# Kernel optimization log

Measured on AMD Instinct MI355X. Metric: run time of the kernel, lower is better.

## Reference

```python
import jax, jax.numpy as jnp
import numpy as np

B, C, H, W, T = 2, 96, 64, 64, 64
NH = 8  # num_heads
WS = 2  # window size per axis (2,2,2)


def setup_inputs() -> dict:
    key = jax.random.key(0)
    ks = jax.random.split(key, 9)
    s = lambda fan_in: 1.0 / np.sqrt(fan_in)
    return {
        "x": jax.random.normal(ks[0], (B, C, H, W, T), dtype=jnp.float32),
        # linear weights stored [in, out] (transposed vs torch nn.Linear)
        "qkv_w": jax.random.normal(ks[1], (C, 3 * C), dtype=jnp.float32) * s(C),
        "qkv_b": jax.random.normal(ks[2], (3 * C,), dtype=jnp.float32) * 0.01,
        "merge_w": jax.random.normal(ks[3], (C, C), dtype=jnp.float32) * s(C),
        "merge_b": jax.random.normal(ks[4], (C,), dtype=jnp.float32) * 0.01,
        "w1": jax.random.normal(ks[5], (2 * C, C), dtype=jnp.float32) * s(2 * C),
        "b1": jax.random.normal(ks[6], (C,), dtype=jnp.float32) * 0.01,
        "w2": jax.random.normal(ks[7], (C, C), dtype=jnp.float32) * s(C),
        "b2": jax.random.normal(ks[8], (C,), dtype=jnp.float32) * 0.01,
    }


def reference(x, qkv_w, qkv_b, merge_w, merge_b, w1, b1, w2, b2):
    b, c, h, w, t = x.shape
    hd = c // NH
    scale = hd ** -0.5
    n = WS * WS * WS  # 8 tokens per window

    xp = jnp.transpose(x, (0, 2, 3, 4, 1))  # [B,H,W,T,C]
    # window partition -> [B*nWin, 8, C]
    xw = xp.reshape(b, h // WS, WS, w // WS, WS, t // WS, WS, c)
    xw = jnp.transpose(xw, (0, 1, 3, 5, 2, 4, 6, 7)).reshape(-1, n, c)

    # windowed MHSA
    qkv = (xw @ qkv_w + qkv_b).reshape(-1, n, 3, NH, hd)
    q, k, v = jnp.moveaxis(qkv, 2, 0)  # each [Bw, n, NH, hd]
    attn = jax.nn.softmax(jnp.einsum('bnhd,bmhd->bhnm', q * scale, k), axis=-1)
    msg = jnp.einsum('bhnm,bmhd->bnhd', attn, v).reshape(-1, n, c)
    msg = msg @ merge_w + merge_b

    # window reverse -> [B,H,W,T,C]
    msg = msg.reshape(b, h // WS, w // WS, t // WS, WS, WS, WS, c)
    msg = jnp.transpose(msg, (0, 1, 4, 2, 5, 3, 6, 7)).reshape(b, h, w, t, c)

    # concat residual path + MLP (GELU exact, matching torch nn.GELU default)
    xt = xp.reshape(b, h * w * t, c)
    mt = msg.reshape(b, h * w * t, c)
    hmid = jax.nn.gelu(jnp.concatenate([xt, mt], axis=-1) @ w1 + b1, approximate=False)
    out = hmid @ w2 + b2
    return jnp.transpose(out.reshape(b, h, w, t, c), (0, 4, 1, 2, 3))
```

## Files before the change

kernel.cpp:

```cpp
#include <hip/hip_runtime.h>
#include <math.h>

typedef short bf16x8 __attribute__((ext_vector_type(8)));
typedef float f32x4 __attribute__((ext_vector_type(4)));

#define SCALE_Q 0.28867513459481287f

__device__ __forceinline__ ushort f2bf(float f) {
  union { float f; unsigned int i; } v; v.f = f;
  unsigned int x = v.i;
  return (ushort)((x + 0x7fffu + ((x >> 16) & 1u)) >> 16);
}
__device__ __forceinline__ float bf2f(ushort u) {
  union { unsigned int i; float f; } v; v.i = ((unsigned int)u) << 16; return v.f;
}
__device__ __forceinline__ float bfLo(unsigned int d) {
  union { unsigned int i; float f; } v; v.i = d << 16; return v.f;
}
__device__ __forceinline__ float bfHi(unsigned int d) {
  union { unsigned int i; float f; } v; v.i = d & 0xffff0000u; return v.f;
}

__global__ void swizzle_w(const float* __restrict__ qkv_w,
                          const float* __restrict__ merge_w,
                          const float* __restrict__ merge_b,
                          const float* __restrict__ w1,
                          const float* __restrict__ b1,
                          const float* __restrict__ w2,
                          ushort* __restrict__ ws) {
  int g = blockIdx.x * 256 + threadIdx.x;
  if (g < 6912) {
    int tile = g >> 6, lane = g & 63;
    float vals[8];
    if (tile < 54) {
      int rem = tile % 18;
      int c0 = (tile / 18) * 96 + (rem / 3) * 16, k0 = (rem % 3) * 32;
      int n = c0 + (lane & 15), kb = k0 + (lane >> 4) * 8;
      float s = (tile < 18) ? SCALE_Q : 1.0f;
#pragma unroll
      for (int j = 0; j < 8; ++j) vals[j] = qkv_w[(size_t)(kb + j) * 288 + n] * s;
    } else if (tile < 72) {
      int rem = tile - 54;
      int c0 = (rem / 3) * 16, k0 = (rem % 3) * 32;
      int n = c0 + (lane & 15), kb = k0 + (lane >> 4) * 8;
#pragma unroll
      for (int j = 0; j < 8; ++j) vals[j] = w1[(size_t)(kb + j) * 96 + n];
    } else if (tile < 90) {
      int rem = tile - 72;
      int c0 = (rem / 3) * 16, k0 = (rem % 3) * 32;
      int n = c0 + (lane & 15), kb = k0 + (lane >> 4) * 8;
      float acc[8] = {0, 0, 0, 0, 0, 0, 0, 0};
      for (int m = 0; m < 96; ++m) {
        float wr = w1[(size_t)(96 + m) * 96 + n];
#pragma unroll
        for (int j = 0; j < 8; ++j) acc[j] += merge_w[(size_t)(kb + j) * 96 + m] * wr;
      }
#pragma unroll
      for (int j = 0; j < 8; ++j) vals[j] = acc[j];
    } else {
      int rem = tile - 90;
      int c0 = (rem / 3) * 16, k0 = (rem % 3) * 32;
      int n = c0 + (lane & 15), kb = k0 + (lane >> 4) * 8;
#pragma unroll
      for (int j = 0; j < 8; ++j) vals[j] = w2[(size_t)(kb + j) * 96 + n];
    }
    ushort tmp[8];
#pragma unroll
    for (int j = 0; j < 8; ++j) tmp[j] = f2bf(vals[j]);
    *(uint4*)(ws + tile * 512 + lane * 8) = *(const uint4*)tmp;
  } else if (g < 7008) {
    int n = g - 6912;
    float s = b1[n];
    for (int m = 0; m < 96; ++m) s += merge_b[m] * w1[(size_t)(96 + m) * 96 + n];
    ((float*)(ws + 55296))[n] = s;
  }
}

#define KPAD 104
#define QPAD 68
#define OPAD 65
__global__ __launch_bounds__(256, 3) void swin_mfma(
    const float* __restrict__ x,
    const float* __restrict__ qkv_b, const float* __restrict__ b2,
    const ushort* __restrict__ wsw, float* __restrict__ out) {
  __shared__ __align__(16) ushort R[288 * QPAD];

  const int tid = threadIdx.x, bid = blockIdx.x;
  const int t0 = bid & 3, w0 = (bid >> 2) & 31, h0 = (bid >> 7) & 31, b = bid >> 12;
  const int lane = tid & 63, wave = tid >> 6;
  const int mrow = lane & 15, quad = lane >> 4;
  const int arow = (wave * 16 + mrow) * KPAD + quad * 8;
  const int tokb = wave * 16 + quad * 4;
  const float* foldb = (const float*)(wsw + 55296);

  for (int i = tid; i < 1536; i += 256) {
    int q = i & 3, dw = (i >> 2) & 1, dh = (i >> 3) & 1, c = i >> 4;
    size_t g = ((((size_t)b * 96 + c) * 64 + h0 * 2 + dh) * 64 + w0 * 2 + dw) * 64 + t0 * 16 + q * 4;
    float4 v = *(const float4*)(x + g);
    float vv[4] = {v.x, v.y, v.z, v.w};
    int base = dh * 4 + dw * 2;
#pragma unroll
    for (int j = 0; j < 4; ++j) {
      int tl = q * 4 + j;
      R[((tl >> 1) * 8 + base + (tl & 1)) * KPAD + c] = f2bf(vv[j]);
    }
  }
  __syncthreads();

  bf16x8 aX[3];
#pragma unroll
  for (int kt = 0; kt < 3; ++kt)
    aX[kt] = *(const bf16x8*)(R + arow + kt * 32);
  __syncthreads();

  for (int cn = 0; cn < 3; ++cn) {
#pragma unroll
    for (int nt = 0; nt < 6; ++nt) {
      int col = cn * 96 + nt * 16 + mrow;
      float bias = qkv_b[col];
      if (cn == 0) bias *= SCALE_Q;
      f32x4 acc = {bias, bias, bias, bias};
#pragma unroll
      for (int kt = 0; kt < 3; ++kt) {
        bf16x8 bf = *(const bf16x8*)(wsw + (size_t)(cn * 18 + nt * 3 + kt) * 512 + lane * 8);
        acc = __builtin_amdgcn_mfma_f32_16x16x32_bf16(aX[kt], bf, acc, 0, 0, 0);
      }
#pragma unroll
      for (int r = 0; r < 4; ++r) R[col * QPAD + tokb + r] = f2bf(acc[r]);
    }
  }
  __syncthreads();

  {
    const int win = tid >> 5, head = (tid >> 2) & 7, r2 = (tid & 3) * 2;
    const ushort* Qb = R + (head * 12) * QPAD + win * 8;
    const ushort* Kb = R + (96 + head * 12) * QPAD + win * 8;
    const ushort* Vb = R + (192 + head * 12) * QPAD + win * 8;
    float q0[12], q1[12];
#pragma unroll
    for (int d = 0; d < 12; ++d) {
      unsigned int qq = *(const unsigned int*)(Qb + d * QPAD + r2);
      q0[d] = bfLo(qq);
      q1[d] = bfHi(qq);
    }
    float s0[8] = {0, 0, 0, 0, 0, 0, 0, 0}, s1[8] = {0, 0, 0, 0, 0, 0, 0, 0};
#pragma unroll
    for (int d = 0; d < 12; ++d) {
      uint2 ka = *(const uint2*)(Kb + d * QPAD);
      uint2 kc = *(const uint2*)(Kb + d * QPAD + 4);
      float kf[8] = {bfLo(ka.x), bfHi(ka.x), bfLo(ka.y), bfHi(ka.y),
                     bfLo(kc.x), bfHi(kc.x), bfLo(kc.y), bfHi(kc.y)};
#pragma unroll
      for (int m = 0; m < 8; ++m) { s0[m] += q0[d] * kf[m]; s1[m] += q1[d] * kf[m]; }
    }
    float mx0 = fmaxf(fmaxf(fmaxf(s0[0], s0[1]), fmaxf(s0[2], s0[3])),
                      fmaxf(fmaxf(s0[4], s0[5]), fmaxf(s0[6], s0[7])));
    float mx1 = fmaxf(fmaxf(fmaxf(s1[0], s1[1]), fmaxf(s1[2], s1[3])),
                      fmaxf(fmaxf(s1[4], s1[5]), fmaxf(s1[6], s1[7])));
    float sum0 = 0.f, sum1 = 0.f;
#pragma unroll
    for (int m = 0; m < 8; ++m) {
      s0[m] = __expf(s0[m] - mx0); sum0 += s0[m];
      s1[m] = __expf(s1[m] - mx1); sum1 += s1[m];
    }
    float inv0 = 1.0f / sum0, inv1 = 1.0f / sum1;
    float o0[12], o1[12];
#pragma unroll
    for (int d = 0; d < 12; ++d) {
      uint2 va = *(const uint2*)(Vb + d * QPAD);
      uint2 vc = *(const uint2*)(Vb + d * QPAD + 4);
      float vf[8] = {bfLo(va.x), bfHi(va.x), bfLo(va.y), bfHi(va.y),
                     bfLo(vc.x), bfHi(vc.x), bfLo(vc.y), bfHi(vc.y)};
      float a0 = 0.f, a1 = 0.f;
#pragma unroll
      for (int m = 0; m < 8; ++m) { a0 += s0[m] * vf[m]; a1 += s1[m] * vf[m]; }
      o0[d] = a0 * inv0; o1[d] = a1 * inv1;
    }
    __syncthreads();
    int tr = win * 8 + r2;
#pragma unroll
    for (int d = 0; d < 12; ++d) {
      R[tr * KPAD + head * 12 + d] = f2bf(o0[d]);
      R[(tr + 1) * KPAD + head * 12 + d] = f2bf(o1[d]);
    }
  }
  __syncthreads();

  {
    bf16x8 aM2[3];
#pragma unroll
    for (int kt = 0; kt < 3; ++kt) aM2[kt] = *(const bf16x8*)(R + arow + kt * 32);
#pragma unroll
    for (int nt = 0; nt < 6; ++nt) {
      int col = nt * 16 + mrow;
      float bias = foldb[col];
      f32x4 acc = {bias, bias, bias, bias};
#pragma unroll
      for (int kt = 0; kt < 3; ++kt) {
        bf16x8 bf = *(const bf16x8*)(wsw + (size_t)(54 + nt * 3 + kt) * 512 + lane * 8);
        acc = __builtin_amdgcn_mfma_f32_16x16x32_bf16(aX[kt], bf, acc, 0, 0, 0);
      }
#pragma unroll
      for (int kt = 0; kt < 3; ++kt) {
        bf16x8 bf = *(const bf16x8*)(wsw + (size_t)(72 + nt * 3 + kt) * 512 + lane * 8);
        acc = __builtin_amdgcn_mfma_f32_16x16x32_bf16(aM2[kt], bf, acc, 0, 0, 0);
      }
#pragma unroll
      for (int r = 0; r < 4; ++r) {
        float h = acc[r];
        float gel = 0.5f * h * (1.0f + erff(h * 0.70710678118654752f));
        R[6656 + (tokb + r) * KPAD + col] = f2bf(gel);
      }
    }
  }
  __syncthreads();

  {
    bf16x8 aH[3];
#pragma unroll
    for (int kt = 0; kt < 3; ++kt) aH[kt] = *(const bf16x8*)(R + 6656 + arow + kt * 32);
#pragma unroll
    for (int nt = 0; nt < 6; ++nt) {
      int col = nt * 16 + mrow;
      float bias = b2[col];
      f32x4 acc = {bias, bias, bias, bias};
#pragma unroll
      for (int kt = 0; kt < 3; ++kt) {
        bf16x8 bf = *(const bf16x8*)(wsw + (size_t)(90 + nt * 3 + kt) * 512 + lane * 8);
        acc = __builtin_amdgcn_mfma_f32_16x16x32_bf16(aH[kt], bf, acc, 0, 0, 0);
      }
#pragma unroll
      for (int r = 0; r < 4; ++r) R[col * OPAD + tokb + r] = f2bf(acc[r]);
    }
  }
  __syncthreads();

  for (int i = tid; i < 1536; i += 256) {
    int q = i & 3, dw = (i >> 2) & 1, dh = (i >> 3) & 1, c = i >> 4;
    float vv[4];
#pragma unroll
    for (int j = 0; j < 4; ++j) {
      int tl = q * 4 + j;
      vv[j] = bf2f(R[c * OPAD + (tl >> 1) * 8 + dh * 4 + dw * 2 + (tl & 1)]);
    }
    float4 v = {vv[0], vv[1], vv[2], vv[3]};
    size_t g = ((((size_t)b * 96 + c) * 64 + h0 * 2 + dh) * 64 + w0 * 2 + dw) * 64 + t0 * 16 + q * 4;
    *(float4*)(out + g) = v;
  }
}

extern "C" void kernel_launch(void* const* d_in, const int* in_sizes, int n_in,
                              void* d_out, int out_size, void* d_ws, size_t ws_size,
                              hipStream_t stream) {
  const float* x = (const float*)d_in[0];
  const float* qkv_w = (const float*)d_in[1];
  const float* qkv_b = (const float*)d_in[2];
  const float* merge_w = (const float*)d_in[3];
  const float* merge_b = (const float*)d_in[4];
  const float* w1 = (const float*)d_in[5];
  const float* b1 = (const float*)d_in[6];
  const float* w2 = (const float*)d_in[7];
  const float* b2 = (const float*)d_in[8];
  ushort* wsw = (ushort*)d_ws;
  swizzle_w<<<dim3(28), dim3(256), 0, stream>>>(qkv_w, merge_w, merge_b, w1, b1, w2, wsw);
  swin_mfma<<<dim3(8192), dim3(256), 0, stream>>>(
      x, qkv_b, b2, wsw, (float*)d_out);
}
```

Baseline: 553.3 us.

## Split each workgroup into single-wave blocks and drop block-level barriers

Each former 256-thread block, covering 8 windows, becomes four 64-thread single-wave blocks that each handle 2 windows, i.e. 16 tokens. Because all shared-memory traffic now stays within one wave, the __syncthreads barriers become compiler-only memory fences, and the shared buffer shrinks to about 11.5 KB so more blocks can be resident. The block index is remapped so the four sibling waves sharing an input row are launched together. The cost is narrower 16-byte global loads per row, four times as many blocks to schedule, and reliance on in-wave LDS ordering with no hardware barrier.

```diff
diff --git a/kernel.cpp b/kernel.cpp
--- a/kernel.cpp
+++ b/kernel.cpp
@@ -20,6 +20,7 @@
 __device__ __forceinline__ float bfHi(unsigned int d) {
   union { unsigned int i; float f; } v; v.i = d & 0xffff0000u; return v.f;
 }
+#define PHASE_FENCE() asm volatile("" ::: "memory")
 
 __global__ void swizzle_w(const float* __restrict__ qkv_w,
                           const float* __restrict__ merge_w,
@@ -76,42 +77,45 @@
   }
 }
 
-#define KPAD 104
-#define QPAD 68
-#define OPAD 65
-__global__ __launch_bounds__(256, 3) void swin_mfma(
+#define XSTR 104
+#define QSTR 20
+#define HMID 1664
+#define OUTR 3840
+__global__ __launch_bounds__(64, 4) void swin_mfma(
     const float* __restrict__ x,
     const float* __restrict__ qkv_b, const float* __restrict__ b2,
     const ushort* __restrict__ wsw, float* __restrict__ out) {
-  __shared__ __align__(16) ushort R[288 * QPAD];
+  __shared__ __align__(16) ushort R[5760];
 
   const int tid = threadIdx.x, bid = blockIdx.x;
-  const int t0 = bid & 3, w0 = (bid >> 2) & 31, h0 = (bid >> 7) & 31, b = bid >> 12;
-  const int lane = tid & 63, wave = tid >> 6;
-  const int mrow = lane & 15, quad = lane >> 4;
-  const int arow = (wave * 16 + mrow) * KPAD + quad * 8;
-  const int tokb = wave * 16 + quad * 4;
+  const int lo3 = bid & 7, wv = (bid >> 3) & 3, hi = bid >> 5;
+  const int old = hi * 8 + lo3;
+  const int t0 = old & 3, w0 = (old >> 2) & 31, h0 = (old >> 7) & 31, b = old >> 12;
+  const int mrow = tid & 15, quad = tid >> 4;
+  const int arow = mrow * XSTR + quad * 8;
+  const int tokb = quad * 4;
   const float* foldb = (const float*)(wsw + 55296);
 
-  for (int i = tid; i < 1536; i += 256) {
-    int q = i & 3, dw = (i >> 2) & 1, dh = (i >> 3) & 1, c = i >> 4;
-    size_t g = ((((size_t)b * 96 + c) * 64 + h0 * 2 + dh) * 64 + w0 * 2 + dw) * 64 + t0 * 16 + q * 4;
+  for (int k = 0; k < 6; ++k) {
+    int item = tid + k * 64;
+    int c = item >> 2, dh = (item >> 1) & 1, dw = item & 1;
+    int base = dh * 4 + dw * 2;
+    size_t g = ((((size_t)b * 96 + c) * 64 + h0 * 2 + dh) * 64 + w0 * 2 + dw) * 64 + t0 * 16 + wv * 4;
     float4 v = *(const float4*)(x + g);
     float vv[4] = {v.x, v.y, v.z, v.w};
-    int base = dh * 4 + dw * 2;
 #pragma unroll
     for (int j = 0; j < 4; ++j) {
-      int tl = q * 4 + j;
-      R[((tl >> 1) * 8 + base + (tl & 1)) * KPAD + c] = f2bf(vv[j]);
-    }
-  }
-  __syncthreads();
+      int tokloc = (j >> 1) * 8 + base + (j & 1);
+      R[tokloc * XSTR + c] = f2bf(vv[j]);
+    }
+  }
+  PHASE_FENCE();
 
   bf16x8 aX[3];
 #pragma unroll
   for (int kt = 0; kt < 3; ++kt)
     aX[kt] = *(const bf16x8*)(R + arow + kt * 32);
-  __syncthreads();
+  PHASE_FENCE();
 
   for (int cn = 0; cn < 3; ++cn) {
 #pragma unroll
@@ -122,34 +126,36 @@
       f32x4 acc = {bias, bias, bias, bias};
 #pragma unroll
       for (int kt = 0; kt < 3; ++kt) {
-        bf16x8 bf = *(const bf16x8*)(wsw + (size_t)(cn * 18 + nt * 3 + kt) * 512 + lane * 8);
+        bf16x8 bf = *(const bf16x8*)(wsw + (size_t)(cn * 18 + nt * 3 + kt) * 512 + tid * 8);
         acc = __builtin_amdgcn_mfma_f32_16x16x32_bf16(aX[kt], bf, acc, 0, 0, 0);
       }
 #pragma unroll
-      for (int r = 0; r < 4; ++r) R[col * QPAD + tokb + r] = f2bf(acc[r]);
-    }
-  }
-  __syncthreads();
+      for (int r = 0; r < 4; ++r) R[col * QSTR + tokb + r] = f2bf(acc[r]);
+    }
+  }
+  PHASE_FENCE();
 
   {
-    const int win = tid >> 5, head = (tid >> 2) & 7, r2 = (tid & 3) * 2;
-    const ushort* Qb = R + (head * 12) * QPAD + win * 8;
-    const ushort* Kb = R + (96 + head * 12) * QPAD + win * 8;
-    const ushort* Vb = R + (192 + head * 12) * QPAD + win * 8;
+    const int winl = tid >> 5, head = (tid >> 2) & 7, r2 = (tid & 3) * 2;
+    const ushort* Qb = R + (head * 12) * QSTR + winl * 8;
+    const ushort* Kb = R + (96 + head * 12) * QSTR + winl * 8;
+    const ushort* Vb = R + (192 + head * 12) * QSTR + winl * 8;
     float q0[12], q1[12];
 #pragma unroll
     for (int d = 0; d < 12; ++d) {
-      unsigned int qq = *(const unsigned int*)(Qb + d * QPAD + r2);
+      unsigned int qq = *(const unsigned int*)(Qb + d * QSTR + r2);
       q0[d] = bfLo(qq);
       q1[d] = bfHi(qq);
     }
     float s0[8] = {0, 0, 0, 0, 0, 0, 0, 0}, s1[8] = {0, 0, 0, 0, 0, 0, 0, 0};
 #pragma unroll
     for (int d = 0; d < 12; ++d) {
-      uint2 ka = *(const uint2*)(Kb + d * QPAD);
-      uint2 kc = *(const uint2*)(Kb + d * QPAD + 4);
-      float kf[8] = {bfLo(ka.x), bfHi(ka.x), bfLo(ka.y), bfHi(ka.y),
-                     bfLo(kc.x), bfHi(kc.x), bfLo(kc.y), bfHi(kc.y)};
+      unsigned int ka = *(const unsigned int*)(Kb + d * QSTR);
+      unsigned int kb2 = *(const unsigned int*)(Kb + d * QSTR + 2);
+      unsigned int kc = *(const unsigned int*)(Kb + d * QSTR + 4);
+      unsigned int kd = *(const unsigned int*)(Kb + d * QSTR + 6);
+      float kf[8] = {bfLo(ka), bfHi(ka), bfLo(kb2), bfHi(kb2),
+                     bfLo(kc), bfHi(kc), bfLo(kd), bfHi(kd)};
 #pragma unroll
       for (int m = 0; m < 8; ++m) { s0[m] += q0[d] * kf[m]; s1[m] += q1[d] * kf[m]; }
     }
@@ -167,24 +173,26 @@
     float o0[12], o1[12];
 #pragma unroll
     for (int d = 0; d < 12; ++d) {
-      uint2 va = *(const uint2*)(Vb + d * QPAD);
-      uint2 vc = *(const uint2*)(Vb + d * QPAD + 4);
-      float vf[8] = {bfLo(va.x), bfHi(va.x), bfLo(va.y), bfHi(va.y),
-                     bfLo(vc.x), bfHi(vc.x), bfLo(vc.y), bfHi(vc.y)};
+      unsigned int va = *(const unsigned int*)(Vb + d * QSTR);
+      unsigned int vb2 = *(const unsigned int*)(Vb + d * QSTR + 2);
+      unsigned int vc = *(const unsigned int*)(Vb + d * QSTR + 4);
+      unsigned int vd = *(const unsigned int*)(Vb + d * QSTR + 6);
+      float vf[8] = {bfLo(va), bfHi(va), bfLo(vb2), bfHi(vb2),
+                     bfLo(vc), bfHi(vc), bfLo(vd), bfHi(vd)};
       float a0 = 0.f, a1 = 0.f;
 #pragma unroll
       for (int m = 0; m < 8; ++m) { a0 += s0[m] * vf[m]; a1 += s1[m] * vf[m]; }
       o0[d] = a0 * inv0; o1[d] = a1 * inv1;
     }
-    __syncthreads();
-    int tr = win * 8 + r2;
-#pragma unroll
-    for (int d = 0; d < 12; ++d) {
-      R[tr * KPAD + head * 12 + d] = f2bf(o0[d]);
-      R[(tr + 1) * KPAD + head * 12 + d] = f2bf(o1[d]);
-    }
-  }
-  __syncthreads();
+    PHASE_FENCE();
+    int tr = winl * 8 + r2;
+#pragma unroll
+    for (int d = 0; d < 12; ++d) {
+      R[tr * XSTR + head * 12 + d] = f2bf(o0[d]);
+      R[(tr + 1) * XSTR + head * 12 + d] = f2bf(o1[d]);
+    }
+  }
+  PHASE_FENCE();
 
   {
     bf16x8 aM2[3];
@@ -197,28 +205,28 @@
       f32x4 acc = {bias, bias, bias, bias};
 #pragma unroll
       for (int kt = 0; kt < 3; ++kt) {
-        bf16x8 bf = *(const bf16x8*)(wsw + (size_t)(54 + nt * 3 + kt) * 512 + lane * 8);
+        bf16x8 bf = *(const bf16x8*)(wsw + (size_t)(54 + nt * 3 + kt) * 512 + tid * 8);
         acc = __builtin_amdgcn_mfma_f32_16x16x32_bf16(aX[kt], bf, acc, 0, 0, 0);
       }
 #pragma unroll
       for (int kt = 0; kt < 3; ++kt) {
-        bf16x8 bf = *(const bf16x8*)(wsw + (size_t)(72 + nt * 3 + kt) * 512 + lane * 8);
+        bf16x8 bf = *(const bf16x8*)(wsw + (size_t)(72 + nt * 3 + kt) * 512 + tid * 8);
         acc = __builtin_amdgcn_mfma_f32_16x16x32_bf16(aM2[kt], bf, acc, 0, 0, 0);
       }
 #pragma unroll
       for (int r = 0; r < 4; ++r) {
         float h = acc[r];
         float gel = 0.5f * h * (1.0f + erff(h * 0.70710678118654752f));
-        R[6656 + (tokb + r) * KPAD + col] = f2bf(gel);
-      }
-    }
-  }
-  __syncthreads();
+        R[HMID + (tokb + r) * XSTR + col] = f2bf(gel);
+      }
+    }
+  }
+  PHASE_FENCE();
 
   {
     bf16x8 aH[3];
 #pragma unroll
-    for (int kt = 0; kt < 3; ++kt) aH[kt] = *(const bf16x8*)(R + 6656 + arow + kt * 32);
+    for (int kt = 0; kt < 3; ++kt) aH[kt] = *(const bf16x8*)(R + HMID + arow + kt * 32);
 #pragma unroll
     for (int nt = 0; nt < 6; ++nt) {
       int col = nt * 16 + mrow;
@@ -226,25 +234,23 @@
       f32x4 acc = {bias, bias, bias, bias};
 #pragma unroll
       for (int kt = 0; kt < 3; ++kt) {
-        bf16x8 bf = *(const bf16x8*)(wsw + (size_t)(90 + nt * 3 + kt) * 512 + lane * 8);
+        bf16x8 bf = *(const bf16x8*)(wsw + (size_t)(90 + nt * 3 + kt) * 512 + tid * 8);
         acc = __builtin_amdgcn_mfma_f32_16x16x32_bf16(aH[kt], bf, acc, 0, 0, 0);
       }
 #pragma unroll
-      for (int r = 0; r < 4; ++r) R[col * OPAD + tokb + r] = f2bf(acc[r]);
-    }
-  }
-  __syncthreads();
-
-  for (int i = tid; i < 1536; i += 256) {
-    int q = i & 3, dw = (i >> 2) & 1, dh = (i >> 3) & 1, c = i >> 4;
-    float vv[4];
-#pragma unroll
-    for (int j = 0; j < 4; ++j) {
-      int tl = q * 4 + j;
-      vv[j] = bf2f(R[c * OPAD + (tl >> 1) * 8 + dh * 4 + dw * 2 + (tl & 1)]);
-    }
-    float4 v = {vv[0], vv[1], vv[2], vv[3]};
-    size_t g = ((((size_t)b * 96 + c) * 64 + h0 * 2 + dh) * 64 + w0 * 2 + dw) * 64 + t0 * 16 + q * 4;
+      for (int r = 0; r < 4; ++r) R[OUTR + col * QSTR + tokb + r] = f2bf(acc[r]);
+    }
+  }
+  PHASE_FENCE();
+
+  for (int k = 0; k < 6; ++k) {
+    int item = tid + k * 64;
+    int c = item >> 2, dh = (item >> 1) & 1, dw = item & 1;
+    int base = dh * 4 + dw * 2;
+    unsigned int p0 = *(const unsigned int*)(R + OUTR + c * QSTR + base);
+    unsigned int p1 = *(const unsigned int*)(R + OUTR + c * QSTR + 8 + base);
+    float4 v = {bfLo(p0), bfHi(p0), bfLo(p1), bfHi(p1)};
+    size_t g = ((((size_t)b * 96 + c) * 64 + h0 * 2 + dh) * 64 + w0 * 2 + dw) * 64 + t0 * 16 + wv * 4;
     *(float4*)(out + g) = v;
   }
 }
@@ -263,6 +269,6 @@
   const float* b2 = (const float*)d_in[8];
   ushort* wsw = (ushort*)d_ws;
   swizzle_w<<<dim3(28), dim3(256), 0, stream>>>(qkv_w, merge_w, merge_b, w1, b1, w2, wsw);
-  swin_mfma<<<dim3(8192), dim3(256), 0, stream>>>(
+  swin_mfma<<<dim3(32768), dim3(64), 0, stream>>>(
       x, qkv_b, b2, wsw, (float*)d_out);
 }
```

Result: slower. 779.3 us (+40.9%).
